# Performance work log

Measured on AMD Instinct MI355X. Metric: run time of the kernel, lower is better.

The kernel has to match this reference:

```python
import jax, jax.numpy as jnp
import numpy as np

NUM_EXPERTS = 8
TOP_K = 2


def setup_inputs() -> dict:
    key = jax.random.key(0)
    k0, k1, k2, k3, k4 = jax.random.split(key, 5)
    T, D, F, E = 4096, 2048, 4096, NUM_EXPERTS  # tokens, hidden, intermediate, experts
    s_in = 1.0 / np.sqrt(D).astype(np.float32)
    s_mid = 1.0 / np.sqrt(F).astype(np.float32)
    return {
        "hidden_states": jax.random.normal(k0, (T, D), jnp.float32),
        "gate_w": jax.random.normal(k1, (D, E), jnp.float32) * s_in,   # router gate (no bias)
        "w1": jax.random.normal(k2, (E, D, F), jnp.float32) * s_in,     # expert gate proj
        "w3": jax.random.normal(k3, (E, D, F), jnp.float32) * s_in,     # expert up proj
        "w2": jax.random.normal(k4, (E, F, D), jnp.float32) * s_mid,    # expert down proj
    }


def reference(hidden_states, gate_w, w1, w3, w2):
    x = hidden_states  # [T, D] (original flattens any leading dims)
    # Router: logits in fp32 (router_logits.float()), softmax over ALL experts,
    # take top-k WITHOUT renormalization (renormalize=False).
    logits = (x @ gate_w).astype(jnp.float32)            # [T, E]
    probs = jax.nn.softmax(logits, axis=-1)              # [T, E]
    topk_w, topk_i = jax.lax.top_k(probs, TOP_K)         # [T, K]
    # Dense combine weights: zero for non-selected experts. [T, E]
    combine = jnp.sum(
        jax.nn.one_hot(topk_i, NUM_EXPERTS, dtype=x.dtype) * topk_w[..., None],
        axis=1,
    )

    # SwiGLU experts, vmapped over the expert axis (fixed, small E).
    def expert_fn(w1e, w3e, w2e):
        return (jax.nn.silu(x @ w1e) * (x @ w3e)) @ w2e  # [T, D]

    expert_out = jax.vmap(expert_fn)(w1, w3, w2)         # [E, T, D]
    return jnp.einsum("te,etd->td", combine, expert_out)  # [T, D]
```

## Files before the change

kernel.cpp:

```cpp
#include <hip/hip_runtime.h>
#include <hip/hip_bf16.h>

#define TK 4096
#define DD 2048
#define FF 4096
#define NE 8
#define BM 128
#define BN 128
#define BKR 32
#define BKP 64

typedef __attribute__((ext_vector_type(8))) short bf16x8;
typedef __attribute__((ext_vector_type(4))) short bf16x4;
typedef __attribute__((ext_vector_type(4))) float f32x4;

__device__ __forceinline__ unsigned short f2bf(float f) {
  return __builtin_bit_cast(unsigned short, __float2bfloat16(f));
}

__device__ __forceinline__ void gl16(const unsigned short* g, unsigned short* l) {
  __builtin_amdgcn_global_load_lds(
      (const __attribute__((address_space(1))) unsigned int*)g,
      (__attribute__((address_space(3))) unsigned int*)l, 16, 0, 0);
}

#define VMCNT(n) asm volatile("s_waitcnt vmcnt(" #n ")" ::: "memory")
#define SBAR()   __builtin_amdgcn_s_barrier()

__device__ __forceinline__ int g_swz(int row) { return ((row >> 1) & 3) ^ ((row >> 3) & 3); }
__device__ __forceinline__ int swzoff(int row, int bir) {
  return row * 64 + ((((bir >> 4) ^ g_swz(row)) & 3) << 4) + (bir & 15);
}
__device__ __forceinline__ int permB(int f) {
  return (f & 0x60) | ((f & 3) << 3) | ((f >> 2) & 7);
}

__global__ void k_router(const float* __restrict__ x, const float* __restrict__ gw,
                         int* __restrict__ cnt, int* __restrict__ ltok,
                         float* __restrict__ lw, unsigned short* __restrict__ xb) {
  int tok = (blockIdx.x * blockDim.x + threadIdx.x) >> 6;
  int lane = threadIdx.x & 63;
  if (tok >= TK) return;
  const float* xr = x + (size_t)tok * DD;
  float a0=0,a1=0,a2=0,a3=0,a4=0,a5=0,a6=0,a7=0;
  for (int p = 0; p < DD / 256; ++p) {
    int d0 = p * 256 + lane * 4;
    f32x4 xv = *(const f32x4*)(xr + d0);
    if (xb) {
      bf16x4 t;
      t[0] = (short)f2bf(xv[0]); t[1] = (short)f2bf(xv[1]);
      t[2] = (short)f2bf(xv[2]); t[3] = (short)f2bf(xv[3]);
      *(bf16x4*)(xb + (size_t)tok * DD + d0) = t;
    }
#pragma unroll
    for (int j = 0; j < 4; ++j) {
      float xs = xv[j];
      const f32x4* g = (const f32x4*)(gw + (size_t)(d0 + j) * NE);
      f32x4 g0 = g[0], g1 = g[1];
      a0 += xs * g0[0]; a1 += xs * g0[1]; a2 += xs * g0[2]; a3 += xs * g0[3];
      a4 += xs * g1[0]; a5 += xs * g1[1]; a6 += xs * g1[2]; a7 += xs * g1[3];
    }
  }
#pragma unroll
  for (int s = 32; s > 0; s >>= 1) {
    a0 += __shfl_xor(a0, s, 64); a1 += __shfl_xor(a1, s, 64);
    a2 += __shfl_xor(a2, s, 64); a3 += __shfl_xor(a3, s, 64);
    a4 += __shfl_xor(a4, s, 64); a5 += __shfl_xor(a5, s, 64);
    a6 += __shfl_xor(a6, s, 64); a7 += __shfl_xor(a7, s, 64);
  }
  if (lane == 0) {
    float p_[NE] = {a0, a1, a2, a3, a4, a5, a6, a7};
    float m = p_[0];
#pragma unroll
    for (int e = 1; e < NE; ++e) m = fmaxf(m, p_[e]);
    float ssum = 0.f;
#pragma unroll
    for (int e = 0; e < NE; ++e) { p_[e] = __expf(p_[e] - m); ssum += p_[e]; }
    float inv = 1.f / ssum;
    int i1 = 0; float b1 = p_[0];
#pragma unroll
    for (int e = 1; e < NE; ++e) if (p_[e] > b1) { b1 = p_[e]; i1 = e; }
    int i2 = -1; float b2 = -1.f;
#pragma unroll
    for (int e = 0; e < NE; ++e) if (e != i1 && p_[e] > b2) { b2 = p_[e]; i2 = e; }
    int s1 = atomicAdd(&cnt[i1], 1);
    ltok[i1 * TK + s1] = tok; lw[i1 * TK + s1] = b1 * inv;
    int s2 = atomicAdd(&cnt[i2], 1);
    ltok[i2 * TK + s2] = tok; lw[i2 * TK + s2] = b2 * inv;
  }
}

__global__ void k_prefix(const int* __restrict__ cnt, int* __restrict__ off) {
  if (threadIdx.x == 0) {
    int a = 0;
#pragma unroll
    for (int e = 0; e < NE; ++e) { off[e] = a; a += cnt[e]; }
    off[NE] = a;
  }
}

__global__ __launch_bounds__(256)
void k_tr(const float* __restrict__ src0, unsigned short* __restrict__ dst0,
          int R, int C) {
  const int e = blockIdx.z;
  const float* src = src0 + (size_t)e * R * C;
  unsigned short* dst = dst0 + (size_t)e * R * C;
  const int tid = threadIdx.x;
  const int w = tid >> 6, lane = tid & 63;
  const int r0 = blockIdx.y * 256 + w * 64 + (lane >> 3) * 8;
  const int c0 = blockIdx.x * 32 + (lane & 7) * 4;
  f32x4 v[8];
#pragma unroll
  for (int j = 0; j < 8; ++j) v[j] = *(const f32x4*)(src + (size_t)(r0 + j) * C + c0);
#pragma unroll
  for (int jc = 0; jc < 4; ++jc) {
    bf16x8 o;
#pragma unroll
    for (int j = 0; j < 8; ++j) o[j] = (short)f2bf(v[j][jc]);
    *(bf16x8*)(dst + (size_t)(c0 + jc) * R + r0) = o;
  }
}


__global__ __launch_bounds__(256, 2)
void k_gemm1g(const unsigned short* __restrict__ xb, const unsigned short* __restrict__ w1t,
              const unsigned short* __restrict__ w3t, const int* __restrict__ cnt,
              const int* __restrict__ off, const int* __restrict__ ltok,
              const float* __restrict__ lw, unsigned short* __restrict__ H) {
  const int e = blockIdx.z;
  const int ce = cnt[e];
  const int m0 = blockIdx.y * BM;
  if (m0 >= ce) return;
  const int n0 = blockIdx.x * BN;
  const int tid = threadIdx.x, lane = tid & 63, w = tid >> 6;
  const int wr = w >> 1, wc = w & 1;
  const unsigned short* W1 = w1t + (size_t)e * FF * DD;
  const unsigned short* W3 = w3t + (size_t)e * FF * DD;
  const int base = off[e];

  __shared__ __align__(16) unsigned short As[BM * BKP];
  __shared__ __align__(16) unsigned short B1s[2][BM * BKP];
  __shared__ __align__(16) unsigned short B3s[2][BM * BKP];

  const int swz8 = ((lane & 7) ^ ((lane >> 3) & 7)) * 8;
  const unsigned short *aSrc[4], *b1Src[4], *b3Src[4];
#pragma unroll
  for (int i = 0; i < 4; ++i) {
    int row = w * 32 + i * 8 + (lane >> 3);
    int gm = m0 + row;
    int tok = (gm < ce) ? ltok[e * TK + gm] : ltok[e * TK];
    aSrc[i]  = xb + (size_t)tok * DD + swz8;
    b1Src[i] = W1 + (size_t)(n0 + row) * DD + swz8;
    b3Src[i] = W3 + (size_t)(n0 + row) * DD + swz8;
  }

  const int kc = lane >> 4;
  int aOff[4][2], bOff[4][2];
#pragma unroll
  for (int m = 0; m < 4; ++m) {
    int row = wr * 64 + m * 16 + (lane & 15);
#pragma unroll
    for (int kk = 0; kk < 2; ++kk) {
      int c = kk * 4 + kc;
      aOff[m][kk] = row * 128 + ((c ^ (row & 7)) << 4);
    }
  }
#pragma unroll
  for (int n = 0; n < 4; ++n) {
    int row = wc * 64 + n * 16 + (lane & 15);
#pragma unroll
    for (int kk = 0; kk < 2; ++kk) {
      int c = kk * 4 + kc;
      bOff[n][kk] = row * 128 + ((c ^ (row & 7)) << 4);
    }
  }

  f32x4 acc1[4][4], acc3[4][4];
#pragma unroll
  for (int m = 0; m < 4; ++m)
#pragma unroll
    for (int n = 0; n < 4; ++n)
#pragma unroll
      for (int j = 0; j < 4; ++j) { acc1[m][n][j] = 0.f; acc3[m][n][j] = 0.f; }

  auto STAGE_A = [&]() {
#pragma unroll
    for (int i = 0; i < 4; ++i) {
      gl16(aSrc[i], &As[(w * 4 + i) * 512]);
      aSrc[i] += BKP;
    }
  };
  auto STAGE_B = [&](int buf) {
#pragma unroll
    for (int i = 0; i < 4; ++i) {
      const int seg = w * 4 + i;
      gl16(b1Src[i], &B1s[buf][seg * 512]);
      gl16(b3Src[i], &B3s[buf][seg * 512]);
      b1Src[i] += BKP; b3Src[i] += BKP;
    }
  };
  auto COMPUTE = [&](int buf) {
#pragma unroll
    for (int kk = 0; kk < 2; ++kk) {
      bf16x8 af[4];
#pragma unroll
      for (int m = 0; m < 4; ++m) af[m] = *(const bf16x8*)((const char*)As + aOff[m][kk]);
#pragma unroll
      for (int n = 0; n < 4; ++n) {
        bf16x8 b1 = *(const bf16x8*)((const char*)B1s[buf] + bOff[n][kk]);
        bf16x8 b3 = *(const bf16x8*)((const char*)B3s[buf] + bOff[n][kk]);
#pragma unroll
        for (int m = 0; m < 4; ++m) {
          acc1[m][n] = __builtin_amdgcn_mfma_f32_16x16x32_bf16(af[m], b1, acc1[m][n], 0, 0, 0);
          acc3[m][n] = __builtin_amdgcn_mfma_f32_16x16x32_bf16(af[m], b3, acc3[m][n], 0, 0, 0);
        }
      }
    }
  };

  const int NT = DD / BKP;
  STAGE_A();
  STAGE_B(0);
  int b = 0;
  for (int kt = 0; kt < NT - 1; ++kt) {
    STAGE_B(b ^ 1);
    VMCNT(8);
    SBAR();
    COMPUTE(b);
    SBAR();
    STAGE_A();
    b ^= 1;
  }
  VMCNT(0);
  SBAR();
  COMPUTE(b);

#pragma unroll
  for (int m = 0; m < 4; ++m) {
    const int rbase = wr * 64 + m * 16 + ((lane >> 4) << 2);
    float wts[4]; bool val[4];
#pragma unroll
    for (int j = 0; j < 4; ++j) {
      int r = m0 + rbase + j;
      val[j] = r < ce;
      wts[j] = val[j] ? lw[e * TK + r] : 0.f;
    }
#pragma unroll
    for (int n = 0; n < 4; ++n) {
      const int col = n0 + wc * 64 + n * 16 + (lane & 15);
#pragma unroll
      for (int j = 0; j < 4; ++j) {
        if (!val[j]) continue;
        float s1 = acc1[m][n][j], s3 = acc3[m][n][j];
        float h = s1 / (1.f + __expf(-s1)) * s3 * wts[j];
        H[(size_t)(base + m0 + rbase + j) * FF + col] = f2bf(h);
      }
    }
  }
}

__global__ __launch_bounds__(256, 3)
void k_gemm2g(const unsigned short* __restrict__ H, const unsigned short* __restrict__ w2t,
              const int* __restrict__ cnt, const int* __restrict__ off,
              const int* __restrict__ ltok, float* __restrict__ out) {
  const int e = blockIdx.z;
  const int ce = cnt[e];
  const int m0 = blockIdx.y * BM;
  if (m0 >= ce) return;
  const int n0 = blockIdx.x * BN;
  const int tid = threadIdx.x, lane = tid & 63, w = tid >> 6;
  const int wr = w >> 1, wc = w & 1;
  const unsigned short* W2 = w2t + (size_t)e * DD * FF;
  const int base = off[e];

  __shared__ __align__(16) unsigned short As[BM * BKP];
  __shared__ __align__(16) unsigned short Bs[2][BM * BKP];

  const int swz8 = ((lane & 7) ^ ((lane >> 3) & 7)) * 8;
  const unsigned short *aSrc[4], *bSrc[4];
#pragma unroll
  for (int i = 0; i < 4; ++i) {
    int row = w * 32 + i * 8 + (lane >> 3);
    int gm = m0 + row;
    int hr = (gm < ce) ? gm : 0;
    aSrc[i] = H + (size_t)(base + hr) * FF + swz8;
    bSrc[i] = W2 + (size_t)(n0 + row) * FF + swz8;
  }

  const int kc = lane >> 4;
  int aOff[4][2], bOff[4][2];
#pragma unroll
  for (int m = 0; m < 4; ++m) {
    int row = wr * 64 + m * 16 + (lane & 15);
#pragma unroll
    for (int kk = 0; kk < 2; ++kk) {
      int c = kk * 4 + kc;
      aOff[m][kk] = row * 128 + ((c ^ (row & 7)) << 4);
    }
  }
#pragma unroll
  for (int n = 0; n < 4; ++n) {
    int row = wc * 64 + n * 16 + (lane & 15);
#pragma unroll
    for (int kk = 0; kk < 2; ++kk) {
      int c = kk * 4 + kc;
      bOff[n][kk] = row * 128 + ((c ^ (row & 7)) << 4);
    }
  }

  f32x4 acc[4][4];
#pragma unroll
  for (int m = 0; m < 4; ++m)
#pragma unroll
    for (int n = 0; n < 4; ++n)
#pragma unroll
      for (int j = 0; j < 4; ++j) acc[m][n][j] = 0.f;

  auto STAGE_A = [&]() {
#pragma unroll
    for (int i = 0; i < 4; ++i) {
      gl16(aSrc[i], &As[(w * 4 + i) * 512]);
      aSrc[i] += BKP;
    }
  };
  auto STAGE_B = [&](int buf) {
#pragma unroll
    for (int i = 0; i < 4; ++i) {
      gl16(bSrc[i], &Bs[buf][(w * 4 + i) * 512]);
      bSrc[i] += BKP;
    }
  };
  auto COMPUTE = [&](int buf) {
#pragma unroll
    for (int kk = 0; kk < 2; ++kk) {
      bf16x8 af[4];
#pragma unroll
      for (int m = 0; m < 4; ++m) af[m] = *(const bf16x8*)((const char*)As + aOff[m][kk]);
#pragma unroll
      for (int n = 0; n < 4; ++n) {
        bf16x8 bf = *(const bf16x8*)((const char*)Bs[buf] + bOff[n][kk]);
#pragma unroll
        for (int m = 0; m < 4; ++m)
          acc[m][n] = __builtin_amdgcn_mfma_f32_16x16x32_bf16(af[m], bf, acc[m][n], 0, 0, 0);
      }
    }
  };

  const int NT = FF / BKP;
  STAGE_A();
  STAGE_B(0);
  int b = 0;
  for (int kt = 0; kt < NT - 1; ++kt) {
    STAGE_B(b ^ 1);
    VMCNT(4);
    SBAR();
    COMPUTE(b);
    SBAR();
    STAGE_A();
    b ^= 1;
  }
  VMCNT(0);
  SBAR();
  COMPUTE(b);

#pragma unroll
  for (int m = 0; m < 4; ++m) {
    const int rbase = wr * 64 + m * 16 + ((lane >> 4) << 2);
    int toks[4]; bool val[4];
#pragma unroll
    for (int j = 0; j < 4; ++j) {
      int r = m0 + rbase + j;
      val[j] = r < ce;
      toks[j] = val[j] ? ltok[e * TK + r] : 0;
    }
#pragma unroll
    for (int n = 0; n < 4; ++n) {
      const int col = n0 + wc * 64 + n * 16 + (lane & 15);
#pragma unroll
      for (int j = 0; j < 4; ++j)
        if (val[j]) atomicAdd(out + (size_t)toks[j] * DD + col, acc[m][n][j]);
    }
  }
}

__global__ __launch_bounds__(256, 2)
void k_gemm1(const float* __restrict__ x, const float* __restrict__ w1g,
             const float* __restrict__ w3g, const int* __restrict__ cnt,
             const int* __restrict__ off, const int* __restrict__ ltok,
             const float* __restrict__ lw, unsigned short* __restrict__ H) {
  const int e = blockIdx.z;
  const int ce = cnt[e];
  const int m0 = blockIdx.y * BM;
  if (m0 >= ce) return;
  const int n0 = blockIdx.x * BN;
  const int tid = threadIdx.x, lane = tid & 63, wv = tid >> 6;
  const int wr = wv >> 1, wc = wv & 1;
  const float* W1 = w1g + (size_t)e * DD * FF;
  const float* W3 = w3g + (size_t)e * DD * FF;
  const int base = off[e];

  __shared__ unsigned short As[2][BM * BKR];
  __shared__ unsigned short B1s[2][BN * BKR];
  __shared__ unsigned short B3s[2][BN * BKR];

  const int arow = tid >> 1, ah = tid & 1;
  const float* xrow = (m0 + arow < ce) ? (x + (size_t)ltok[e * TK + (m0 + arow)] * DD) : nullptr;
  const int dblk = tid >> 5, fblk = tid & 31;

  const int kb = (lane >> 4) * 16;
  int aOff[4], bOff[4], wAoff[4], wBoff[4];
#pragma unroll
  for (int m = 0; m < 4; ++m) aOff[m] = swzoff(wr * 64 + m * 16 + (lane & 15), kb);
#pragma unroll
  for (int n = 0; n < 4; ++n) bOff[n] = swzoff(permB(wc * 64 + n * 16 + (lane & 15)), kb);
#pragma unroll
  for (int j = 0; j < 4; ++j) {
    wAoff[j] = swzoff(arow, ah * 32 + j * 8);
    wBoff[j] = swzoff(permB(fblk * 4 + j), dblk * 8);
  }

  f32x4 acc1[4][4], acc3[4][4];
#pragma unroll
  for (int m = 0; m < 4; ++m)
#pragma unroll
    for (int n = 0; n < 4; ++n)
#pragma unroll
      for (int j = 0; j < 4; ++j) { acc1[m][n][j] = 0.f; acc3[m][n][j] = 0.f; }

  f32x4 av[4], v1[4], v3[4];

  auto LOAD = [&](int kt) {
    const int k0 = kt * BKR;
#pragma unroll
    for (int j = 0; j < 4; ++j) {
      if (xrow) av[j] = *(const f32x4*)(xrow + k0 + ah * 16 + j * 4);
      else { av[j][0] = 0.f; av[j][1] = 0.f; av[j][2] = 0.f; av[j][3] = 0.f; }
    }
    const float* p1 = W1 + (size_t)(k0 + dblk * 4) * FF + (n0 + fblk * 4);
    const float* p3 = W3 + (size_t)(k0 + dblk * 4) * FF + (n0 + fblk * 4);
#pragma unroll
    for (int r = 0; r < 4; ++r) {
      v1[r] = *(const f32x4*)(p1 + (size_t)r * FF);
      v3[r] = *(const f32x4*)(p3 + (size_t)r * FF);
    }
  };
  auto STORE = [&](int buf) {
#pragma unroll
    for (int j = 0; j < 4; ++j) {
      bf16x4 t;
      t[0] = (short)f2bf(av[j][0]); t[1] = (short)f2bf(av[j][1]);
      t[2] = (short)f2bf(av[j][2]); t[3] = (short)f2bf(av[j][3]);
      *(bf16x4*)((char*)As[buf] + wAoff[j]) = t;
    }
#pragma unroll
    for (int j = 0; j < 4; ++j) {
      bf16x4 t1, t3;
      t1[0] = (short)f2bf(v1[0][j]); t1[1] = (short)f2bf(v1[1][j]);
      t1[2] = (short)f2bf(v1[2][j]); t1[3] = (short)f2bf(v1[3][j]);
      t3[0] = (short)f2bf(v3[0][j]); t3[1] = (short)f2bf(v3[1][j]);
      t3[2] = (short)f2bf(v3[2][j]); t3[3] = (short)f2bf(v3[3][j]);
      *(bf16x4*)((char*)B1s[buf] + wBoff[j]) = t1;
      *(bf16x4*)((char*)B3s[buf] + wBoff[j]) = t3;
    }
  };

  LOAD(0); STORE(0);
  int cur = 0;
  const int NT = DD / BKR;
  for (int kt = 0; kt < NT; ++kt) {
    if (kt + 1 < NT) LOAD(kt + 1);
    __syncthreads();
    bf16x8 af[4];
#pragma unroll
    for (int m = 0; m < 4; ++m) af[m] = *(const bf16x8*)((const char*)As[cur] + aOff[m]);
#pragma unroll
    for (int n = 0; n < 4; ++n) {
      bf16x8 b1 = *(const bf16x8*)((const char*)B1s[cur] + bOff[n]);
      bf16x8 b3 = *(const bf16x8*)((const char*)B3s[cur] + bOff[n]);
#pragma unroll
      for (int m = 0; m < 4; ++m) {
        acc1[m][n] = __builtin_amdgcn_mfma_f32_16x16x32_bf16(af[m], b1, acc1[m][n], 0, 0, 0);
        acc3[m][n] = __builtin_amdgcn_mfma_f32_16x16x32_bf16(af[m], b3, acc3[m][n], 0, 0, 0);
      }
    }
    if (kt + 1 < NT) STORE(cur ^ 1);
    cur ^= 1;
  }

#pragma unroll
  for (int m = 0; m < 4; ++m) {
    const int rbase = wr * 64 + m * 16 + ((lane >> 4) << 2);
    float wts[4]; bool val[4];
#pragma unroll
    for (int j = 0; j < 4; ++j) {
      int r = m0 + rbase + j;
      val[j] = r < ce;
      wts[j] = val[j] ? lw[e * TK + r] : 0.f;
    }
#pragma unroll
    for (int n = 0; n < 4; ++n) {
      const int col = n0 + wc * 64 + n * 16 + (lane & 15);
#pragma unroll
      for (int j = 0; j < 4; ++j) {
        if (!val[j]) continue;
        float s1 = acc1[m][n][j], s3 = acc3[m][n][j];
        float h = s1 / (1.f + __expf(-s1)) * s3 * wts[j];
        H[(size_t)(base + m0 + rbase + j) * FF + col] = f2bf(h);
      }
    }
  }
}

__global__ __launch_bounds__(256, 2)
void k_gemm2(const unsigned short* __restrict__ H, const float* __restrict__ w2g,
             const int* __restrict__ cnt, const int* __restrict__ off,
             const int* __restrict__ ltok, float* __restrict__ out) {
  const int e = blockIdx.z;
  const int ce = cnt[e];
  const int m0 = blockIdx.y * BM;
  if (m0 >= ce) return;
  const int n0 = blockIdx.x * BN;
  const int tid = threadIdx.x, lane = tid & 63, wv = tid >> 6;
  const int wr = wv >> 1, wc = wv & 1;
  const float* W2 = w2g + (size_t)e * FF * DD;
  const int base = off[e];

  __shared__ unsigned short As[2][BM * BKR];
  __shared__ unsigned short Bs[2][BN * BKR];

  const int arow = tid >> 1, ah = tid & 1;
  const bool aval = (m0 + arow) < ce;
  const unsigned short* hrow = H + (size_t)(base + m0 + arow) * FF;
  const int kblk = tid >> 5, nblk = tid & 31;

  const int kb = (lane >> 4) * 16;
  int aOff[4], bOff[4], wAoff[2], wBoff[4];
#pragma unroll
  for (int m = 0; m < 4; ++m) aOff[m] = swzoff(wr * 64 + m * 16 + (lane & 15), kb);
#pragma unroll
  for (int n = 0; n < 4; ++n) bOff[n] = swzoff(permB(wc * 64 + n * 16 + (lane & 15)), kb);
#pragma unroll
  for (int j = 0; j < 2; ++j) wAoff[j] = swzoff(arow, ah * 32 + j * 16);
#pragma unroll
  for (int j = 0; j < 4; ++j) wBoff[j] = swzoff(permB(nblk * 4 + j), kblk * 8);

  f32x4 acc[4][4];
#pragma unroll
  for (int m = 0; m < 4; ++m)
#pragma unroll
    for (int n = 0; n < 4; ++n)
#pragma unroll
      for (int j = 0; j < 4; ++j) acc[m][n][j] = 0.f;

  bf16x8 av2[2];
  f32x4 wv2[4];

  auto LOAD = [&](int kt) {
    const int k0 = kt * BKR;
#pragma unroll
    for (int j = 0; j < 2; ++j) {
      if (aval) av2[j] = *(const bf16x8*)(hrow + k0 + ah * 16 + j * 8);
      else {
#pragma unroll
        for (int q = 0; q < 8; ++q) av2[j][q] = 0;
      }
    }
    const float* p = W2 + (size_t)(k0 + kblk * 4) * DD + (n0 + nblk * 4);
#pragma unroll
    for (int r = 0; r < 4; ++r) wv2[r] = *(const f32x4*)(p + (size_t)r * DD);
  };
  auto STORE = [&](int buf) {
#pragma unroll
    for (int j = 0; j < 2; ++j) *(bf16x8*)((char*)As[buf] + wAoff[j]) = av2[j];
#pragma unroll
    for (int j = 0; j < 4; ++j) {
      bf16x4 t;
      t[0] = (short)f2bf(wv2[0][j]); t[1] = (short)f2bf(wv2[1][j]);
      t[2] = (short)f2bf(wv2[2][j]); t[3] = (short)f2bf(wv2[3][j]);
      *(bf16x4*)((char*)Bs[buf] + wBoff[j]) = t;
    }
  };

  LOAD(0); STORE(0);
  int cur = 0;
  const int NT = FF / BKR;
  for (int kt = 0; kt < NT; ++kt) {
    if (kt + 1 < NT) LOAD(kt + 1);
    __syncthreads();
    bf16x8 af[4];
#pragma unroll
    for (int m = 0; m < 4; ++m) af[m] = *(const bf16x8*)((const char*)As[cur] + aOff[m]);
#pragma unroll
    for (int n = 0; n < 4; ++n) {
      bf16x8 bf = *(const bf16x8*)((const char*)Bs[cur] + bOff[n]);
#pragma unroll
      for (int m = 0; m < 4; ++m)
        acc[m][n] = __builtin_amdgcn_mfma_f32_16x16x32_bf16(af[m], bf, acc[m][n], 0, 0, 0);
    }
    if (kt + 1 < NT) STORE(cur ^ 1);
    cur ^= 1;
  }

#pragma unroll
  for (int m = 0; m < 4; ++m) {
    const int rbase = wr * 64 + m * 16 + ((lane >> 4) << 2);
    int toks[4]; bool val[4];
#pragma unroll
    for (int j = 0; j < 4; ++j) {
      int r = m0 + rbase + j;
      val[j] = r < ce;
      toks[j] = val[j] ? ltok[e * TK + r] : 0;
    }
#pragma unroll
    for (int n = 0; n < 4; ++n) {
      const int col = n0 + wc * 64 + n * 16 + (lane & 15);
#pragma unroll
      for (int j = 0; j < 4; ++j)
        if (val[j]) atomicAdd(out + (size_t)toks[j] * DD + col, acc[m][n][j]);
    }
  }
}

extern "C" void kernel_launch(void* const* d_in, const int* in_sizes, int n_in,
                              void* d_out, int out_size, void* d_ws, size_t ws_size,
                              hipStream_t stream) {
  const float* x  = (const float*)d_in[0];
  const float* gw = (const float*)d_in[1];
  const float* w1 = (const float*)d_in[2];
  const float* w3 = (const float*)d_in[3];
  const float* w2 = (const float*)d_in[4];
  float* out = (float*)d_out;

  char* ws = (char*)d_ws;
  int*   cnt  = (int*)(ws);
  int*   off  = (int*)(ws + 64);
  int*   ltok = (int*)(ws + 256);
  float* lw   = (float*)(ws + 256 + (size_t)NE * TK * 4);

  const size_t SZ_XB = (size_t)TK * DD * 2;
  const size_t SZ_W  = (size_t)NE * DD * FF * 2;
  const size_t SZ_H  = (size_t)2 * TK * FF * 2;
  size_t o = (size_t)1 << 20;
  unsigned short* xb  = (unsigned short*)(ws + o); o += SZ_XB;
  unsigned short* w1t = (unsigned short*)(ws + o); o += SZ_W;
  unsigned short* w3t = (unsigned short*)(ws + o); o += SZ_W;
  unsigned short* w2t = (unsigned short*)(ws + o); o += SZ_W;
  unsigned short* Hg  = (unsigned short*)(ws + o); o += SZ_H;
  const bool full = (ws_size >= o);

  hipMemsetAsync(cnt, 0, 64, stream);
  hipMemsetAsync(d_out, 0, (size_t)out_size * 4, stream);

  if (full) {
    k_router<<<dim3(TK / 4), 256, 0, stream>>>(x, gw, cnt, ltok, lw, xb);
    k_prefix<<<dim3(1), 64, 0, stream>>>(cnt, off);
    k_tr<<<dim3(FF / 32, DD / 256, NE), 256, 0, stream>>>(w1, w1t, DD, FF);
    k_tr<<<dim3(FF / 32, DD / 256, NE), 256, 0, stream>>>(w3, w3t, DD, FF);
    k_tr<<<dim3(DD / 32, FF / 256, NE), 256, 0, stream>>>(w2, w2t, FF, DD);
    k_gemm1g<<<dim3(FF / BN, TK / BM, NE), 256, 0, stream>>>(xb, w1t, w3t, cnt, off, ltok, lw, Hg);
    k_gemm2g<<<dim3(DD / BN, TK / BM, NE), 256, 0, stream>>>(Hg, w2t, cnt, off, ltok, out);
  } else {
    unsigned short* H = (unsigned short*)(ws + ((size_t)1 << 20));
    if (ws_size < ((size_t)1 << 20) + SZ_H) return;
    k_router<<<dim3(TK / 4), 256, 0, stream>>>(x, gw, cnt, ltok, lw, (unsigned short*)nullptr);
    k_prefix<<<dim3(1), 64, 0, stream>>>(cnt, off);
    k_gemm1<<<dim3(FF / BN, TK / BM, NE), 256, 0, stream>>>(x, w1, w3, cnt, off, ltok, lw, H);
    k_gemm2<<<dim3(DD / BN, TK / BM, NE), 256, 0, stream>>>(H, w2, cnt, off, ltok, out);
  }
}
```

Before: 938.3 us.

## Replace atomic scatter in down-proj with bf16 staging plus gather-combine kernel

```diff
diff --git a/kernel.cpp b/kernel.cpp
--- a/kernel.cpp
+++ b/kernel.cpp
@@ -7,6 +7,7 @@
 #define NE 8
 #define BM 128
 #define BN 128
+#define BN2 256
 #define BKR 32
 #define BKP 64
 
@@ -16,6 +17,9 @@
 
 __device__ __forceinline__ unsigned short f2bf(float f) {
   return __builtin_bit_cast(unsigned short, __float2bfloat16(f));
+}
+__device__ __forceinline__ float bf2f(unsigned short u) {
+  return __builtin_bit_cast(float, (unsigned)u << 16);
 }
 
 __device__ __forceinline__ void gl16(const unsigned short* g, unsigned short* l) {
@@ -37,7 +41,8 @@
 
 __global__ void k_router(const float* __restrict__ x, const float* __restrict__ gw,
                          int* __restrict__ cnt, int* __restrict__ ltok,
-                         float* __restrict__ lw, unsigned short* __restrict__ xb) {
+                         float* __restrict__ lw, unsigned short* __restrict__ xb,
+                         int2* __restrict__ t2s) {
   int tok = (blockIdx.x * blockDim.x + threadIdx.x) >> 6;
   int lane = threadIdx.x & 63;
   if (tok >= TK) return;
@@ -87,6 +92,7 @@
     ltok[i1 * TK + s1] = tok; lw[i1 * TK + s1] = b1 * inv;
     int s2 = atomicAdd(&cnt[i2], 1);
     ltok[i2 * TK + s2] = tok; lw[i2 * TK + s2] = b2 * inv;
+    if (t2s) t2s[tok] = make_int2(i1 * TK + s1, i2 * TK + s2);
   }
 }
 
@@ -119,6 +125,28 @@
     for (int j = 0; j < 8; ++j) o[j] = (short)f2bf(v[j][jc]);
     *(bf16x8*)(dst + (size_t)(c0 + jc) * R + r0) = o;
   }
+}
+
+__global__ __launch_bounds__(256)
+void k_comb(const unsigned short* __restrict__ O, const int2* __restrict__ t2s,
+            const int* __restrict__ off, float* __restrict__ out) {
+  const int idx = blockIdx.x * 256 + threadIdx.x;
+  const int t = idx >> 8;
+  const int d0 = (idx & 255) * 8;
+  const int2 v = t2s[t];
+  const int s1 = off[v.x >> 12] + (v.x & (TK - 1));
+  const int s2 = off[v.y >> 12] + (v.y & (TK - 1));
+  bf16x8 a = *(const bf16x8*)(O + (size_t)s1 * DD + d0);
+  bf16x8 b = *(const bf16x8*)(O + (size_t)s2 * DD + d0);
+  f32x4 r0, r1;
+#pragma unroll
+  for (int j = 0; j < 4; ++j) {
+    r0[j] = bf2f((unsigned short)a[j]) + bf2f((unsigned short)b[j]);
+    r1[j] = bf2f((unsigned short)a[j + 4]) + bf2f((unsigned short)b[j + 4]);
+  }
+  float* o = out + (size_t)t * DD + d0;
+  *(f32x4*)o = r0;
+  *(f32x4*)(o + 4) = r1;
 }
 
 
@@ -259,36 +287,40 @@
   }
 }
 
-__global__ __launch_bounds__(256, 3)
+__global__ __launch_bounds__(256, 2)
 void k_gemm2g(const unsigned short* __restrict__ H, const unsigned short* __restrict__ w2t,
               const int* __restrict__ cnt, const int* __restrict__ off,
-              const int* __restrict__ ltok, float* __restrict__ out) {
+              unsigned short* __restrict__ O) {
   const int e = blockIdx.z;
   const int ce = cnt[e];
   const int m0 = blockIdx.y * BM;
   if (m0 >= ce) return;
-  const int n0 = blockIdx.x * BN;
+  const int n0 = blockIdx.x * BN2;
   const int tid = threadIdx.x, lane = tid & 63, w = tid >> 6;
   const int wr = w >> 1, wc = w & 1;
   const unsigned short* W2 = w2t + (size_t)e * DD * FF;
   const int base = off[e];
 
   __shared__ __align__(16) unsigned short As[BM * BKP];
-  __shared__ __align__(16) unsigned short Bs[2][BM * BKP];
+  __shared__ __align__(16) unsigned short Bs[2][BN2 * BKP];
 
   const int swz8 = ((lane & 7) ^ ((lane >> 3) & 7)) * 8;
-  const unsigned short *aSrc[4], *bSrc[4];
+  const unsigned short *aSrc[4], *bSrc[8];
 #pragma unroll
   for (int i = 0; i < 4; ++i) {
     int row = w * 32 + i * 8 + (lane >> 3);
     int gm = m0 + row;
     int hr = (gm < ce) ? gm : 0;
     aSrc[i] = H + (size_t)(base + hr) * FF + swz8;
+  }
+#pragma unroll
+  for (int i = 0; i < 8; ++i) {
+    int row = w * 64 + i * 8 + (lane >> 3);
     bSrc[i] = W2 + (size_t)(n0 + row) * FF + swz8;
   }
 
   const int kc = lane >> 4;
-  int aOff[4][2], bOff[4][2];
+  int aOff[4][2], bOff[8][2];
 #pragma unroll
   for (int m = 0; m < 4; ++m) {
     int row = wr * 64 + m * 16 + (lane & 15);
@@ -299,8 +331,8 @@
     }
   }
 #pragma unroll
-  for (int n = 0; n < 4; ++n) {
-    int row = wc * 64 + n * 16 + (lane & 15);
+  for (int n = 0; n < 8; ++n) {
+    int row = wc * 128 + n * 16 + (lane & 15);
 #pragma unroll
     for (int kk = 0; kk < 2; ++kk) {
       int c = kk * 4 + kc;
@@ -308,11 +340,11 @@
     }
   }
 
-  f32x4 acc[4][4];
+  f32x4 acc[4][8];
 #pragma unroll
   for (int m = 0; m < 4; ++m)
 #pragma unroll
-    for (int n = 0; n < 4; ++n)
+    for (int n = 0; n < 8; ++n)
 #pragma unroll
       for (int j = 0; j < 4; ++j) acc[m][n][j] = 0.f;
 
@@ -325,8 +357,8 @@
   };
   auto STAGE_B = [&](int buf) {
 #pragma unroll
-    for (int i = 0; i < 4; ++i) {
-      gl16(bSrc[i], &Bs[buf][(w * 4 + i) * 512]);
+    for (int i = 0; i < 8; ++i) {
+      gl16(bSrc[i], &Bs[buf][(w * 8 + i) * 512]);
       bSrc[i] += BKP;
     }
   };
@@ -337,7 +369,7 @@
 #pragma unroll
       for (int m = 0; m < 4; ++m) af[m] = *(const bf16x8*)((const char*)As + aOff[m][kk]);
 #pragma unroll
-      for (int n = 0; n < 4; ++n) {
+      for (int n = 0; n < 8; ++n) {
         bf16x8 bf = *(const bf16x8*)((const char*)Bs[buf] + bOff[n][kk]);
 #pragma unroll
         for (int m = 0; m < 4; ++m)
@@ -352,7 +384,7 @@
   int b = 0;
   for (int kt = 0; kt < NT - 1; ++kt) {
     STAGE_B(b ^ 1);
-    VMCNT(4);
+    VMCNT(8);
     SBAR();
     COMPUTE(b);
     SBAR();
@@ -366,19 +398,14 @@
 #pragma unroll
   for (int m = 0; m < 4; ++m) {
     const int rbase = wr * 64 + m * 16 + ((lane >> 4) << 2);
-    int toks[4]; bool val[4];
-#pragma unroll
-    for (int j = 0; j < 4; ++j) {
-      int r = m0 + rbase + j;
-      val[j] = r < ce;
-      toks[j] = val[j] ? ltok[e * TK + r] : 0;
-    }
-#pragma unroll
-    for (int n = 0; n < 4; ++n) {
-      const int col = n0 + wc * 64 + n * 16 + (lane & 15);
-#pragma unroll
-      for (int j = 0; j < 4; ++j)
-        if (val[j]) atomicAdd(out + (size_t)toks[j] * DD + col, acc[m][n][j]);
+#pragma unroll
+    for (int n = 0; n < 8; ++n) {
+      const int col = n0 + wc * 128 + n * 16 + (lane & 15);
+#pragma unroll
+      for (int j = 0; j < 4; ++j) {
+        int r = m0 + rbase + j;
+        if (r < ce) O[(size_t)(base + r) * DD + col] = f2bf(acc[m][n][j]);
+      }
     }
   }
 }
@@ -636,6 +663,7 @@
   int*   off  = (int*)(ws + 64);
   int*   ltok = (int*)(ws + 256);
   float* lw   = (float*)(ws + 256 + (size_t)NE * TK * 4);
+  int2*  t2s  = (int2*)(ws + 512 * 1024);
 
   const size_t SZ_XB = (size_t)TK * DD * 2;
   const size_t SZ_W  = (size_t)NE * DD * FF * 2;
@@ -646,23 +674,26 @@
   unsigned short* w3t = (unsigned short*)(ws + o); o += SZ_W;
   unsigned short* w2t = (unsigned short*)(ws + o); o += SZ_W;
   unsigned short* Hg  = (unsigned short*)(ws + o); o += SZ_H;
+  unsigned short* O   = w1t;
   const bool full = (ws_size >= o);
 
   hipMemsetAsync(cnt, 0, 64, stream);
-  hipMemsetAsync(d_out, 0, (size_t)out_size * 4, stream);
 
   if (full) {
-    k_router<<<dim3(TK / 4), 256, 0, stream>>>(x, gw, cnt, ltok, lw, xb);
+    k_router<<<dim3(TK / 4), 256, 0, stream>>>(x, gw, cnt, ltok, lw, xb, t2s);
     k_prefix<<<dim3(1), 64, 0, stream>>>(cnt, off);
     k_tr<<<dim3(FF / 32, DD / 256, NE), 256, 0, stream>>>(w1, w1t, DD, FF);
     k_tr<<<dim3(FF / 32, DD / 256, NE), 256, 0, stream>>>(w3, w3t, DD, FF);
     k_tr<<<dim3(DD / 32, FF / 256, NE), 256, 0, stream>>>(w2, w2t, FF, DD);
     k_gemm1g<<<dim3(FF / BN, TK / BM, NE), 256, 0, stream>>>(xb, w1t, w3t, cnt, off, ltok, lw, Hg);
-    k_gemm2g<<<dim3(DD / BN, TK / BM, NE), 256, 0, stream>>>(Hg, w2t, cnt, off, ltok, out);
+    k_gemm2g<<<dim3(DD / BN2, TK / BM, NE), 256, 0, stream>>>(Hg, w2t, cnt, off, O);
+    k_comb<<<dim3(TK * DD / 8 / 256), 256, 0, stream>>>(O, t2s, off, out);
   } else {
     unsigned short* H = (unsigned short*)(ws + ((size_t)1 << 20));
     if (ws_size < ((size_t)1 << 20) + SZ_H) return;
-    k_router<<<dim3(TK / 4), 256, 0, stream>>>(x, gw, cnt, ltok, lw, (unsigned short*)nullptr);
+    hipMemsetAsync(d_out, 0, (size_t)out_size * 4, stream);
+    k_router<<<dim3(TK / 4), 256, 0, stream>>>(x, gw, cnt, ltok, lw,
+                                               (unsigned short*)nullptr, (int2*)nullptr);
     k_prefix<<<dim3(1), 64, 0, stream>>>(cnt, off);
     k_gemm1<<<dim3(FF / BN, TK / BM, NE), 256, 0, stream>>>(x, w1, w3, cnt, off, ltok, lw, H);
     k_gemm2<<<dim3(DD / BN, TK / BM, NE), 256, 0, stream>>>(H, w2, cnt, off, ltok, out);
```

New measurement: 976.6 us. +4.1%, slower.
